# Kernel tuning notes

Hardware: AMD Instinct MI355X
Metric: run time of the kernel (lower is better)

The kernel has to match this reference:

```python
import jax, jax.numpy as jnp
import numpy as np

H = 1024        # hidden_size
V = 50257       # output_size (vocab)
L = 50          # max_length (encoder positions)
N_LAYERS = 2    # python loop count over the shared single-layer GRU


def setup_inputs() -> dict:
    key = jax.random.key(0)
    ks = jax.random.split(key, 16)
    s = 0.02
    return {
        "input_ids": jax.random.randint(ks[0], (1,), 0, V),
        "hidden": jax.random.normal(ks[1], (1, 1, H), jnp.float32),
        "encoder_outputs": jax.random.normal(ks[2], (L, H), jnp.float32),
        # learned parameters
        "emb": jax.random.normal(ks[3], (V, H), jnp.float32) * s,
        "attn_w": jax.random.normal(ks[4], (L, 2 * H), jnp.float32) * s,
        "attn_b": jnp.zeros((L,), jnp.float32),
        "comb_w": jax.random.normal(ks[5], (H, 2 * H), jnp.float32) * s,
        "comb_b": jnp.zeros((H,), jnp.float32),
        "w_ih": jax.random.normal(ks[6], (3 * H, H), jnp.float32) * s,
        "w_hh": jax.random.normal(ks[7], (3 * H, H), jnp.float32) * s,
        "b_ih": jnp.zeros((3 * H,), jnp.float32),
        "b_hh": jnp.zeros((3 * H,), jnp.float32),
        "out_w": jax.random.normal(ks[8], (V, H), jnp.float32) * s,
        "out_b": jnp.zeros((V,), jnp.float32),
    }


def _gru_cell(x, h, w_ih, w_hh, b_ih, b_hh):
    # PyTorch GRU gate order: [r, z, n] stacked along dim 0 of (3H, H) weights.
    gx = w_ih @ x + b_ih
    gh = w_hh @ h + b_hh
    r = jax.nn.sigmoid(gx[:H] + gh[:H])
    z = jax.nn.sigmoid(gx[H:2 * H] + gh[H:2 * H])
    n = jnp.tanh(gx[2 * H:] + r * gh[2 * H:])
    return (1.0 - z) * n + z * h


def reference(input_ids, hidden, encoder_outputs, emb, attn_w, attn_b,
              comb_w, comb_b, w_ih, w_hh, b_ih, b_hh, out_w, out_b):
    # batch=1 single decode step; dropout is identity (eval mode)
    embedded = emb[input_ids[0]]                     # [H]
    h = hidden[0, 0]                                 # [H]
    concat = jnp.concatenate([embedded, h])          # [2H]
    attn_weights = jax.nn.softmax(attn_w @ concat + attn_b)   # [L]
    attn_applied = attn_weights @ encoder_outputs    # [H]  (bmm with batch 1)
    output = comb_w @ jnp.concatenate([embedded, attn_applied]) + comb_b  # [H]
    for _ in range(N_LAYERS):                        # shared-weight GRU called twice
        x = jax.nn.relu(output)
        h = _gru_cell(x, h, w_ih, w_hh, b_ih, b_hh)
        output = h
    log_probs = jax.nn.log_softmax(out_w @ output + out_b)    # [V]
    return log_probs[None, :], h[None, None, :], attn_weights[None, :]
```

## Files before the change

### kernel.cpp

```cpp
#include <hip/hip_runtime.h>
#include <hip/hip_bf16.h>

#define H 1024
#define V 50257
#define L 50

__global__ void attn_kernel(const int* __restrict__ input_ids,
                            const float* __restrict__ hidden,
                            const float* __restrict__ enc,
                            const float* __restrict__ emb,
                            const float* __restrict__ attn_w,
                            const float* __restrict__ attn_b,
                            float* __restrict__ ws_emb,
                            float* __restrict__ ws_app,
                            float* __restrict__ out_attnw) {
    __shared__ __align__(16) float s_concat[2 * H];
    __shared__ float s_w[L];
    const int tid = threadIdx.x;
    const int token = input_ids[0];

    const float4* e4 = (const float4*)(emb + (size_t)token * H);
    const float4* h4 = (const float4*)hidden;
    {
        float4 e = e4[tid];
        float4 h = h4[tid];
        ((float4*)s_concat)[tid] = e;
        ((float4*)(s_concat + H))[tid] = h;
        ((float4*)ws_emb)[tid] = e;
    }
    __syncthreads();

    const int wave = tid >> 6, lane = tid & 63;
    for (int l = wave; l < L; l += 4) {
        const float4* r4 = (const float4*)(attn_w + (size_t)l * 2 * H);
        const float4* c4 = (const float4*)s_concat;
        float acc = 0.f;
        for (int k = lane; k < 512; k += 64) {
            float4 a = r4[k], b = c4[k];
            acc += a.x * b.x + a.y * b.y + a.z * b.z + a.w * b.w;
        }
        #pragma unroll
        for (int off = 32; off; off >>= 1) acc += __shfl_down(acc, off);
        if (lane == 0) s_w[l] = acc + attn_b[l];
    }
    __syncthreads();

    if (tid == 0) {
        float m = s_w[0];
        for (int l = 1; l < L; ++l) m = fmaxf(m, s_w[l]);
        float s = 0.f;
        for (int l = 0; l < L; ++l) { s_w[l] = __expf(s_w[l] - m); s += s_w[l]; }
        float inv = 1.f / s;
        for (int l = 0; l < L; ++l) s_w[l] *= inv;
    }
    __syncthreads();
    if (tid < L) out_attnw[tid] = s_w[tid];

    float4 acc = make_float4(0.f, 0.f, 0.f, 0.f);
    for (int l = 0; l < L; ++l) {
        float w = s_w[l];
        float4 v = ((const float4*)(enc + (size_t)l * H))[tid];
        acc.x += w * v.x; acc.y += w * v.y; acc.z += w * v.z; acc.w += w * v.w;
    }
    ((float4*)ws_app)[tid] = acc;
}

__global__ void comb_kernel(const float* __restrict__ comb_w,
                            const float* __restrict__ comb_b,
                            const float* __restrict__ embedded,
                            const float* __restrict__ applied,
                            float* __restrict__ x1) {
    __shared__ __align__(16) float s_c[2 * H];
    const int tid = threadIdx.x;
    ((float4*)s_c)[tid] = ((const float4*)embedded)[tid];
    ((float4*)(s_c + H))[tid] = ((const float4*)applied)[tid];
    __syncthreads();

    const int wave = tid >> 6, lane = tid & 63;
    const int i = blockIdx.x * 4 + wave;
    const float4* r4 = (const float4*)(comb_w + (size_t)i * 2 * H);
    const float4* c4 = (const float4*)s_c;
    float acc = 0.f;
    for (int k = lane; k < 512; k += 64) {
        float4 a = r4[k], b = c4[k];
        acc += a.x * b.x + a.y * b.y + a.z * b.z + a.w * b.w;
    }
    #pragma unroll
    for (int off = 32; off; off >>= 1) acc += __shfl_down(acc, off);
    if (lane == 0) x1[i] = fmaxf(acc + comb_b[i], 0.f);
}

__global__ void gru_kernel(const float* __restrict__ x,
                           const float* __restrict__ hprev,
                           const float* __restrict__ w_ih,
                           const float* __restrict__ w_hh,
                           const float* __restrict__ b_ih,
                           const float* __restrict__ b_hh,
                           float* __restrict__ h_out,
                           float* __restrict__ x_out,
                           float* __restrict__ h_copy)
{
    __shared__ __align__(16) float s_x[H];
    __shared__ __align__(16) float s_h[H];
    const int tid = threadIdx.x;
    ((float4*)s_x)[tid] = ((const float4*)x)[tid];
    ((float4*)s_h)[tid] = ((const float4*)hprev)[tid];
    __syncthreads();

    const int wave = tid >> 6, lane = tid & 63;
    const int i = blockIdx.x * 4 + wave;
    const float4* x4 = (const float4*)s_x;
    const float4* h4 = (const float4*)s_h;
    const float4* wr_x = (const float4*)(w_ih + (size_t)i * H);
    const float4* wz_x = (const float4*)(w_ih + (size_t)(H + i) * H);
    const float4* wn_x = (const float4*)(w_ih + (size_t)(2 * H + i) * H);
    const float4* wr_h = (const float4*)(w_hh + (size_t)i * H);
    const float4* wz_h = (const float4*)(w_hh + (size_t)(H + i) * H);
    const float4* wn_h = (const float4*)(w_hh + (size_t)(2 * H + i) * H);

    float ar = 0.f, az = 0.f, an = 0.f, br = 0.f, bz = 0.f, bn = 0.f;
    for (int k = lane; k < 256; k += 64) {
        float4 xv = x4[k], hv = h4[k], t;
        t = wr_x[k]; ar += t.x * xv.x + t.y * xv.y + t.z * xv.z + t.w * xv.w;
        t = wz_x[k]; az += t.x * xv.x + t.y * xv.y + t.z * xv.z + t.w * xv.w;
        t = wn_x[k]; an += t.x * xv.x + t.y * xv.y + t.z * xv.z + t.w * xv.w;
        t = wr_h[k]; br += t.x * hv.x + t.y * hv.y + t.z * hv.z + t.w * hv.w;
        t = wz_h[k]; bz += t.x * hv.x + t.y * hv.y + t.z * hv.z + t.w * hv.w;
        t = wn_h[k]; bn += t.x * hv.x + t.y * hv.y + t.z * hv.z + t.w * hv.w;
    }
    #pragma unroll
    for (int off = 32; off; off >>= 1) {
        ar += __shfl_down(ar, off); az += __shfl_down(az, off);
        an += __shfl_down(an, off); br += __shfl_down(br, off);
        bz += __shfl_down(bz, off); bn += __shfl_down(bn, off);
    }
    if (lane == 0) {
        float gxr = ar + b_ih[i],         ghr = br + b_hh[i];
        float gxz = az + b_ih[H + i],     ghz = bz + b_hh[H + i];
        float gxn = an + b_ih[2 * H + i], ghn = bn + b_hh[2 * H + i];
        float r = 1.f / (1.f + expf(-(gxr + ghr)));
        float z = 1.f / (1.f + expf(-(gxz + ghz)));
        float n = tanhf(gxn + r * ghn);
        float hn = (1.f - z) * n + z * s_h[i];
        h_out[i] = hn;
        if (x_out) x_out[i] = fmaxf(hn, 0.f);
        if (h_copy) h_copy[i] = hn;
    }
}

__global__ void logits_kernel(const float* __restrict__ out_w,
                              const float* __restrict__ out_b,
                              const float* __restrict__ h,
                              float* __restrict__ logits,
                              float* __restrict__ partials) {
    __shared__ __align__(16) float s_h[H];
    __shared__ float s_part[4];
    const int tid = threadIdx.x;
    ((float4*)s_h)[tid] = ((const float4*)h)[tid];
    __syncthreads();

    const int wave = tid >> 6, lane = tid & 63;
    const float4* h4 = (const float4*)s_h;
    float psum = 0.f;
    #pragma unroll
    for (int rr = 0; rr < 2; ++rr) {
        const int v = blockIdx.x * 8 + wave * 2 + rr;
        if (v < V) {
            const float4* w4 = (const float4*)(out_w + (size_t)v * H);
            float acc = 0.f;
            for (int k = lane; k < 256; k += 64) {
                float4 a = w4[k], b = h4[k];
                acc += a.x * b.x + a.y * b.y + a.z * b.z + a.w * b.w;
            }
            #pragma unroll
            for (int off = 32; off; off >>= 1) acc += __shfl_down(acc, off);
            if (lane == 0) {
                float lg = acc + out_b[v];
                logits[v] = lg;
                psum += expf(lg);
            }
        }
    }
    if (lane == 0) s_part[wave] = psum;
    __syncthreads();
    if (tid == 0) partials[blockIdx.x] = s_part[0] + s_part[1] + s_part[2] + s_part[3];
}

__global__ void lse_kernel(const float* __restrict__ partials, int n,
                           float* __restrict__ lse) {
    __shared__ float red[256];
    const int tid = threadIdx.x;
    float s = 0.f;
    for (int i = tid; i < n; i += 256) s += partials[i];
    red[tid] = s;
    __syncthreads();
    for (int off = 128; off; off >>= 1) {
        if (tid < off) red[tid] += red[tid + off];
        __syncthreads();
    }
    if (tid == 0) *lse = logf(red[0]);
}

__global__ void sub_kernel(const float* __restrict__ logits,
                           const float* __restrict__ lse,
                           float* __restrict__ out) {
    const int v = blockIdx.x * 256 + threadIdx.x;
    if (v < V) out[v] = logits[v] - *lse;
}

extern "C" void kernel_launch(void* const* d_in, const int* in_sizes, int n_in,
                              void* d_out, int out_size, void* d_ws, size_t ws_size,
                              hipStream_t stream) {
    const int*   input_ids = (const int*)d_in[0];
    const float* hidden    = (const float*)d_in[1];
    const float* enc       = (const float*)d_in[2];
    const float* emb       = (const float*)d_in[3];
    const float* attn_w    = (const float*)d_in[4];
    const float* attn_b    = (const float*)d_in[5];
    const float* comb_w    = (const float*)d_in[6];
    const float* comb_b    = (const float*)d_in[7];
    const float* w_ih      = (const float*)d_in[8];
    const float* w_hh      = (const float*)d_in[9];
    const float* b_ih      = (const float*)d_in[10];
    const float* b_hh      = (const float*)d_in[11];
    const float* out_w     = (const float*)d_in[12];
    const float* out_b     = (const float*)d_in[13];

    float* out = (float*)d_out;
    float* ws  = (float*)d_ws;
    float* ws_emb    = ws;
    float* ws_app    = ws + 1024;
    float* ws_x1     = ws + 2048;
    float* ws_h1     = ws + 3072;
    float* ws_x2     = ws + 4096;
    float* ws_h2     = ws + 5120;
    float* ws_logits = ws + 6144;
    float* ws_part   = ws + 6144 + 50432;
    float* ws_lse    = ws_part + 6400;

    const int nblk_logits = (V + 7) / 8;

    attn_kernel<<<1, 256, 0, stream>>>(input_ids, hidden, enc, emb, attn_w, attn_b,
                                       ws_emb, ws_app, out + V + H);
    comb_kernel<<<256, 256, 0, stream>>>(comb_w, comb_b, ws_emb, ws_app, ws_x1);
    gru_kernel<<<256, 256, 0, stream>>>(ws_x1, hidden, w_ih, w_hh, b_ih, b_hh,
                                        ws_h1, ws_x2, nullptr);
    gru_kernel<<<256, 256, 0, stream>>>(ws_x2, ws_h1, w_ih, w_hh, b_ih, b_hh,
                                        ws_h2, nullptr, out + V);
    logits_kernel<<<nblk_logits, 256, 0, stream>>>(out_w, out_b, ws_h2,
                                                   ws_logits, ws_part);
    lse_kernel<<<1, 256, 0, stream>>>(ws_part, nblk_logits, ws_lse);
    sub_kernel<<<(V + 255) / 256, 256, 0, stream>>>(ws_logits, ws_lse, out);
}
```

Baseline: 451.2 us.

## Fuse decoder step into one persistent kernel with grid barriers

Replaces the seven separate kernels (attention, combine, two GRU steps, logits, logsumexp, subtract) with one persistent 256-block kernel that separates phases with atomic-counter grid barriers. Attention scores are spread over 50 blocks instead of one, and logits are written directly to the output then corrected in place. This removes launch gaps and the single-block attention bottleneck, at the cost of relying on all blocks being co-resident and spin-wait barrier overhead.

```diff
diff --git a/kernel.cpp b/kernel.cpp
--- a/kernel.cpp
+++ b/kernel.cpp
@@ -4,208 +4,222 @@
 #define H 1024
 #define V 50257
 #define L 50
-
-__global__ void attn_kernel(const int* __restrict__ input_ids,
-                            const float* __restrict__ hidden,
-                            const float* __restrict__ enc,
-                            const float* __restrict__ emb,
-                            const float* __restrict__ attn_w,
-                            const float* __restrict__ attn_b,
-                            float* __restrict__ ws_emb,
-                            float* __restrict__ ws_app,
-                            float* __restrict__ out_attnw) {
-    __shared__ __align__(16) float s_concat[2 * H];
-    __shared__ float s_w[L];
-    const int tid = threadIdx.x;
+#define NB 256
+#define NT 1024
+
+__device__ inline void gridbar(unsigned* cnt) {
+    __syncthreads();
+    if (threadIdx.x == 0) {
+        __threadfence();
+        atomicAdd(cnt, 1u);
+        while (__hip_atomic_load(cnt, __ATOMIC_ACQUIRE, __HIP_MEMORY_SCOPE_AGENT) < NB)
+            __builtin_amdgcn_s_sleep(2);
+        __threadfence();
+    }
+    __syncthreads();
+}
+
+__global__ __launch_bounds__(NT, 4) void fused_decoder(
+    const int* __restrict__ input_ids, const float* __restrict__ hidden,
+    const float* __restrict__ enc,     const float* __restrict__ emb,
+    const float* __restrict__ attn_w,  const float* __restrict__ attn_b,
+    const float* __restrict__ comb_w,  const float* __restrict__ comb_b,
+    const float* __restrict__ w_ih,    const float* __restrict__ w_hh,
+    const float* __restrict__ b_ih,    const float* __restrict__ b_hh,
+    const float* __restrict__ out_w,   const float* __restrict__ out_b,
+    float* __restrict__ out, float* __restrict__ ws, unsigned* __restrict__ bar)
+{
+    __shared__ float smem[2048 + 192];
+    const int tid  = threadIdx.x;
+    const int bid  = blockIdx.x;
+    const int wave = tid >> 6, lane = tid & 63;
+
+    float* ws_scores = ws;
+    float* ws_app    = ws + 64;
+    float* ws_x1     = ws_app + H;
+    float* ws_h1     = ws_x1 + H;
+    float* ws_x2     = ws_h1 + H;
+    float* ws_h2     = ws_x2 + H;
+    float* ws_part   = ws_h2 + H;
+
     const int token = input_ids[0];
-
-    const float4* e4 = (const float4*)(emb + (size_t)token * H);
-    const float4* h4 = (const float4*)hidden;
-    {
-        float4 e = e4[tid];
-        float4 h = h4[tid];
-        ((float4*)s_concat)[tid] = e;
-        ((float4*)(s_concat + H))[tid] = h;
-        ((float4*)ws_emb)[tid] = e;
-    }
-    __syncthreads();
-
-    const int wave = tid >> 6, lane = tid & 63;
-    for (int l = wave; l < L; l += 4) {
-        const float4* r4 = (const float4*)(attn_w + (size_t)l * 2 * H);
-        const float4* c4 = (const float4*)s_concat;
+    const float* embrow = emb + (size_t)token * H;
+
+    if (bid < L) {
+        const float* arow = attn_w + (size_t)bid * 2 * H;
         float acc = 0.f;
-        for (int k = lane; k < 512; k += 64) {
-            float4 a = r4[k], b = c4[k];
+        if (tid < 512) {
+            float4 a = ((const float4*)arow)[tid];
+            float4 x = (tid < 256) ? ((const float4*)embrow)[tid]
+                                   : ((const float4*)hidden)[tid - 256];
+            acc = a.x * x.x + a.y * x.y + a.z * x.z + a.w * x.w;
+        }
+        #pragma unroll
+        for (int off = 32; off; off >>= 1) acc += __shfl_down(acc, off);
+        if (tid < 512 && lane == 0) smem[wave] = acc;
+        __syncthreads();
+        if (tid == 0) {
+            float s = 0.f;
+            for (int w = 0; w < 8; ++w) s += smem[w];
+            ws_scores[bid] = s + attn_b[bid];
+        }
+    }
+    gridbar(bar + 0 * 16);
+
+    {
+        if (tid == 0) {
+            float m = ws_scores[0];
+            for (int l = 1; l < L; ++l) m = fmaxf(m, ws_scores[l]);
+            float s = 0.f;
+            for (int l = 0; l < L; ++l) { float e = expf(ws_scores[l] - m); smem[l] = e; s += e; }
+            float inv = 1.f / s;
+            for (int l = 0; l < L; ++l) smem[l] *= inv;
+        }
+        __syncthreads();
+        if (tid < 4) {
+            int j = bid * 4 + tid;
+            float acc = 0.f;
+            for (int l = 0; l < L; ++l) acc += smem[l] * enc[l * H + j];
+            ws_app[j] = acc;
+        }
+        if (bid == 0 && tid >= 64 && tid < 64 + L)
+            out[V + H + (tid - 64)] = smem[tid - 64];
+    }
+    gridbar(bar + 1 * 16);
+
+    {
+        float4* sc4 = (float4*)smem;
+        if (tid < 256)      sc4[tid]       = ((const float4*)embrow)[tid];
+        else if (tid < 512) sc4[tid]       = ((const float4*)ws_app)[tid - 256];
+        __syncthreads();
+        int r = bid * 4 + (wave >> 2);
+        int seg = wave & 3;
+        const float4* wr = (const float4*)(comb_w + (size_t)r * 2 * H);
+        float acc = 0.f;
+        #pragma unroll
+        for (int k = 0; k < 2; ++k) {
+            int idx = seg * 128 + k * 64 + lane;
+            float4 a = wr[idx], b = sc4[idx];
             acc += a.x * b.x + a.y * b.y + a.z * b.z + a.w * b.w;
         }
         #pragma unroll
         for (int off = 32; off; off >>= 1) acc += __shfl_down(acc, off);
-        if (lane == 0) s_w[l] = acc + attn_b[l];
-    }
-    __syncthreads();
-
-    if (tid == 0) {
-        float m = s_w[0];
-        for (int l = 1; l < L; ++l) m = fmaxf(m, s_w[l]);
-        float s = 0.f;
-        for (int l = 0; l < L; ++l) { s_w[l] = __expf(s_w[l] - m); s += s_w[l]; }
-        float inv = 1.f / s;
-        for (int l = 0; l < L; ++l) s_w[l] *= inv;
-    }
-    __syncthreads();
-    if (tid < L) out_attnw[tid] = s_w[tid];
-
-    float4 acc = make_float4(0.f, 0.f, 0.f, 0.f);
-    for (int l = 0; l < L; ++l) {
-        float w = s_w[l];
-        float4 v = ((const float4*)(enc + (size_t)l * H))[tid];
-        acc.x += w * v.x; acc.y += w * v.y; acc.z += w * v.z; acc.w += w * v.w;
-    }
-    ((float4*)ws_app)[tid] = acc;
-}
-
-__global__ void comb_kernel(const float* __restrict__ comb_w,
-                            const float* __restrict__ comb_b,
-                            const float* __restrict__ embedded,
-                            const float* __restrict__ applied,
-                            float* __restrict__ x1) {
-    __shared__ __align__(16) float s_c[2 * H];
-    const int tid = threadIdx.x;
-    ((float4*)s_c)[tid] = ((const float4*)embedded)[tid];
-    ((float4*)(s_c + H))[tid] = ((const float4*)applied)[tid];
-    __syncthreads();
-
-    const int wave = tid >> 6, lane = tid & 63;
-    const int i = blockIdx.x * 4 + wave;
-    const float4* r4 = (const float4*)(comb_w + (size_t)i * 2 * H);
-    const float4* c4 = (const float4*)s_c;
-    float acc = 0.f;
-    for (int k = lane; k < 512; k += 64) {
-        float4 a = r4[k], b = c4[k];
-        acc += a.x * b.x + a.y * b.y + a.z * b.z + a.w * b.w;
-    }
-    #pragma unroll
-    for (int off = 32; off; off >>= 1) acc += __shfl_down(acc, off);
-    if (lane == 0) x1[i] = fmaxf(acc + comb_b[i], 0.f);
-}
-
-__global__ void gru_kernel(const float* __restrict__ x,
-                           const float* __restrict__ hprev,
-                           const float* __restrict__ w_ih,
-                           const float* __restrict__ w_hh,
-                           const float* __restrict__ b_ih,
-                           const float* __restrict__ b_hh,
-                           float* __restrict__ h_out,
-                           float* __restrict__ x_out,
-                           float* __restrict__ h_copy)
-{
-    __shared__ __align__(16) float s_x[H];
-    __shared__ __align__(16) float s_h[H];
-    const int tid = threadIdx.x;
-    ((float4*)s_x)[tid] = ((const float4*)x)[tid];
-    ((float4*)s_h)[tid] = ((const float4*)hprev)[tid];
-    __syncthreads();
-
-    const int wave = tid >> 6, lane = tid & 63;
-    const int i = blockIdx.x * 4 + wave;
-    const float4* x4 = (const float4*)s_x;
-    const float4* h4 = (const float4*)s_h;
-    const float4* wr_x = (const float4*)(w_ih + (size_t)i * H);
-    const float4* wz_x = (const float4*)(w_ih + (size_t)(H + i) * H);
-    const float4* wn_x = (const float4*)(w_ih + (size_t)(2 * H + i) * H);
-    const float4* wr_h = (const float4*)(w_hh + (size_t)i * H);
-    const float4* wz_h = (const float4*)(w_hh + (size_t)(H + i) * H);
-    const float4* wn_h = (const float4*)(w_hh + (size_t)(2 * H + i) * H);
-
-    float ar = 0.f, az = 0.f, an = 0.f, br = 0.f, bz = 0.f, bn = 0.f;
-    for (int k = lane; k < 256; k += 64) {
-        float4 xv = x4[k], hv = h4[k], t;
-        t = wr_x[k]; ar += t.x * xv.x + t.y * xv.y + t.z * xv.z + t.w * xv.w;
-        t = wz_x[k]; az += t.x * xv.x + t.y * xv.y + t.z * xv.z + t.w * xv.w;
-        t = wn_x[k]; an += t.x * xv.x + t.y * xv.y + t.z * xv.z + t.w * xv.w;
-        t = wr_h[k]; br += t.x * hv.x + t.y * hv.y + t.z * hv.z + t.w * hv.w;
-        t = wz_h[k]; bz += t.x * hv.x + t.y * hv.y + t.z * hv.z + t.w * hv.w;
-        t = wn_h[k]; bn += t.x * hv.x + t.y * hv.y + t.z * hv.z + t.w * hv.w;
-    }
-    #pragma unroll
-    for (int off = 32; off; off >>= 1) {
-        ar += __shfl_down(ar, off); az += __shfl_down(az, off);
-        an += __shfl_down(an, off); br += __shfl_down(br, off);
-        bz += __shfl_down(bz, off); bn += __shfl_down(bn, off);
-    }
-    if (lane == 0) {
-        float gxr = ar + b_ih[i],         ghr = br + b_hh[i];
-        float gxz = az + b_ih[H + i],     ghz = bz + b_hh[H + i];
-        float gxn = an + b_ih[2 * H + i], ghn = bn + b_hh[2 * H + i];
-        float r = 1.f / (1.f + expf(-(gxr + ghr)));
-        float z = 1.f / (1.f + expf(-(gxz + ghz)));
-        float n = tanhf(gxn + r * ghn);
-        float hn = (1.f - z) * n + z * s_h[i];
-        h_out[i] = hn;
-        if (x_out) x_out[i] = fmaxf(hn, 0.f);
-        if (h_copy) h_copy[i] = hn;
-    }
-}
-
-__global__ void logits_kernel(const float* __restrict__ out_w,
-                              const float* __restrict__ out_b,
-                              const float* __restrict__ h,
-                              float* __restrict__ logits,
-                              float* __restrict__ partials) {
-    __shared__ __align__(16) float s_h[H];
-    __shared__ float s_part[4];
-    const int tid = threadIdx.x;
-    ((float4*)s_h)[tid] = ((const float4*)h)[tid];
-    __syncthreads();
-
-    const int wave = tid >> 6, lane = tid & 63;
-    const float4* h4 = (const float4*)s_h;
-    float psum = 0.f;
-    #pragma unroll
-    for (int rr = 0; rr < 2; ++rr) {
-        const int v = blockIdx.x * 8 + wave * 2 + rr;
-        if (v < V) {
-            const float4* w4 = (const float4*)(out_w + (size_t)v * H);
+        if (lane == 0) smem[2048 + wave] = acc;
+        __syncthreads();
+        if (tid < 4) {
+            int rr = bid * 4 + tid;
+            float s = smem[2048 + tid * 4] + smem[2048 + tid * 4 + 1]
+                    + smem[2048 + tid * 4 + 2] + smem[2048 + tid * 4 + 3];
+            ws_x1[rr] = fmaxf(s + comb_b[rr], 0.f);
+        }
+    }
+    gridbar(bar + 2 * 16);
+
+    for (int layer = 0; layer < 2; ++layer) {
+        const float* x  = (layer == 0) ? ws_x1 : ws_x2;
+        const float* hp = (layer == 0) ? hidden : ws_h1;
+        float* h_out  = (layer == 0) ? ws_h1 : ws_h2;
+        float* x_out  = (layer == 0) ? ws_x2 : nullptr;
+        float* h_copy = (layer == 0) ? nullptr : out + V;
+
+        float4* sx4 = (float4*)smem;
+        float4* sh4 = (float4*)(smem + 1024);
+        if (tid < 256)      sx4[tid]       = ((const float4*)x)[tid];
+        else if (tid < 512) sh4[tid - 256] = ((const float4*)hp)[tid - 256];
+        __syncthreads();
+
+        int r   = bid * 4 + (wave >> 2);
+        int seg = wave & 3;
+        int idx = seg * 64 + lane;
+        float4 xv = sx4[idx], hv = sh4[idx];
+        const float4* m0 = (const float4*)(w_ih + (size_t)r * H);
+        const float4* m1 = (const float4*)(w_ih + (size_t)(H + r) * H);
+        const float4* m2 = (const float4*)(w_ih + (size_t)(2 * H + r) * H);
+        const float4* m3 = (const float4*)(w_hh + (size_t)r * H);
+        const float4* m4 = (const float4*)(w_hh + (size_t)(H + r) * H);
+        const float4* m5 = (const float4*)(w_hh + (size_t)(2 * H + r) * H);
+        float4 t;
+        float a0, a1, a2, a3, a4, a5;
+        t = m0[idx]; a0 = t.x * xv.x + t.y * xv.y + t.z * xv.z + t.w * xv.w;
+        t = m1[idx]; a1 = t.x * xv.x + t.y * xv.y + t.z * xv.z + t.w * xv.w;
+        t = m2[idx]; a2 = t.x * xv.x + t.y * xv.y + t.z * xv.z + t.w * xv.w;
+        t = m3[idx]; a3 = t.x * hv.x + t.y * hv.y + t.z * hv.z + t.w * hv.w;
+        t = m4[idx]; a4 = t.x * hv.x + t.y * hv.y + t.z * hv.z + t.w * hv.w;
+        t = m5[idx]; a5 = t.x * hv.x + t.y * hv.y + t.z * hv.z + t.w * hv.w;
+        #pragma unroll
+        for (int off = 32; off; off >>= 1) {
+            a0 += __shfl_down(a0, off); a1 += __shfl_down(a1, off);
+            a2 += __shfl_down(a2, off); a3 += __shfl_down(a3, off);
+            a4 += __shfl_down(a4, off); a5 += __shfl_down(a5, off);
+        }
+        if (lane == 0) {
+            float* p = smem + 2048 + wave * 8;
+            p[0] = a0; p[1] = a1; p[2] = a2; p[3] = a3; p[4] = a4; p[5] = a5;
+        }
+        __syncthreads();
+        if (tid < 4) {
+            int rr = bid * 4 + tid;
+            float g0 = 0, g1 = 0, g2 = 0, g3 = 0, g4 = 0, g5 = 0;
+            #pragma unroll
+            for (int s = 0; s < 4; ++s) {
+                float* p = smem + 2048 + (tid * 4 + s) * 8;
+                g0 += p[0]; g1 += p[1]; g2 += p[2]; g3 += p[3]; g4 += p[4]; g5 += p[5];
+            }
+            float gxr = g0 + b_ih[rr],         ghr = g3 + b_hh[rr];
+            float gxz = g1 + b_ih[H + rr],     ghz = g4 + b_hh[H + rr];
+            float gxn = g2 + b_ih[2 * H + rr], ghn = g5 + b_hh[2 * H + rr];
+            float rg = 1.f / (1.f + expf(-(gxr + ghr)));
+            float zg = 1.f / (1.f + expf(-(gxz + ghz)));
+            float ng = tanhf(gxn + rg * ghn);
+            float hval = smem[1024 + rr];
+            float hn = (1.f - zg) * ng + zg * hval;
+            h_out[rr] = hn;
+            if (x_out)  x_out[rr]  = fmaxf(hn, 0.f);
+            if (h_copy) h_copy[rr] = hn;
+        }
+        gridbar(bar + (3 + layer) * 16);
+    }
+
+    {
+        float4* sh4 = (float4*)smem;
+        if (tid < 256) sh4[tid] = ((const float4*)ws_h2)[tid];
+        __syncthreads();
+        int gw = bid * 16 + wave;
+        float psum = 0.f;
+        for (int v = gw; v < V; v += 4096) {
+            const float4* wr = (const float4*)(out_w + (size_t)v * H);
             float acc = 0.f;
-            for (int k = lane; k < 256; k += 64) {
-                float4 a = w4[k], b = h4[k];
+            #pragma unroll
+            for (int k = 0; k < 4; ++k) {
+                int idx = k * 64 + lane;
+                float4 a = wr[idx], b = sh4[idx];
                 acc += a.x * b.x + a.y * b.y + a.z * b.z + a.w * b.w;
             }
             #pragma unroll
             for (int off = 32; off; off >>= 1) acc += __shfl_down(acc, off);
             if (lane == 0) {
                 float lg = acc + out_b[v];
-                logits[v] = lg;
+                out[v] = lg;
                 psum += expf(lg);
             }
         }
-    }
-    if (lane == 0) s_part[wave] = psum;
-    __syncthreads();
-    if (tid == 0) partials[blockIdx.x] = s_part[0] + s_part[1] + s_part[2] + s_part[3];
-}
-
-__global__ void lse_kernel(const float* __restrict__ partials, int n,
-                           float* __restrict__ lse) {
-    __shared__ float red[256];
-    const int tid = threadIdx.x;
-    float s = 0.f;
-    for (int i = tid; i < n; i += 256) s += partials[i];
-    red[tid] = s;
-    __syncthreads();
-    for (int off = 128; off; off >>= 1) {
-        if (tid < off) red[tid] += red[tid + off];
-        __syncthreads();
-    }
-    if (tid == 0) *lse = logf(red[0]);
-}
-
-__global__ void sub_kernel(const float* __restrict__ logits,
-                           const float* __restrict__ lse,
-                           float* __restrict__ out) {
-    const int v = blockIdx.x * 256 + threadIdx.x;
-    if (v < V) out[v] = logits[v] - *lse;
+        if (lane == 0) ws_part[gw] = psum;
+    }
+    gridbar(bar + 5 * 16);
+
+    {
+        float s = 0.f;
+        for (int i = tid; i < 4096; i += NT) s += ws_part[i];
+        smem[tid] = s;
+        __syncthreads();
+        for (int off = 512; off; off >>= 1) {
+            if (tid < off) smem[tid] += smem[tid + off];
+            __syncthreads();
+        }
+        float lse = logf(smem[0]);
+        int g = bid * NT + tid;
+        if (g < V) out[g] -= lse;
+    }
 }
 
 extern "C" void kernel_launch(void* const* d_in, const int* in_sizes, int n_in,
@@ -228,27 +242,10 @@
 
     float* out = (float*)d_out;
     float* ws  = (float*)d_ws;
-    float* ws_emb    = ws;
-    float* ws_app    = ws + 1024;
-    float* ws_x1     = ws + 2048;
-    float* ws_h1     = ws + 3072;
-    float* ws_x2     = ws + 4096;
-    float* ws_h2     = ws + 5120;
-    float* ws_logits = ws + 6144;
-    float* ws_part   = ws + 6144 + 50432;
-    float* ws_lse    = ws_part + 6400;
-
-    const int nblk_logits = (V + 7) / 8;
-
-    attn_kernel<<<1, 256, 0, stream>>>(input_ids, hidden, enc, emb, attn_w, attn_b,
-                                       ws_emb, ws_app, out + V + H);
-    comb_kernel<<<256, 256, 0, stream>>>(comb_w, comb_b, ws_emb, ws_app, ws_x1);
-    gru_kernel<<<256, 256, 0, stream>>>(ws_x1, hidden, w_ih, w_hh, b_ih, b_hh,
-                                        ws_h1, ws_x2, nullptr);
-    gru_kernel<<<256, 256, 0, stream>>>(ws_x2, ws_h1, w_ih, w_hh, b_ih, b_hh,
-                                        ws_h2, nullptr, out + V);
-    logits_kernel<<<nblk_logits, 256, 0, stream>>>(out_w, out_b, ws_h2,
-                                                   ws_logits, ws_part);
-    lse_kernel<<<1, 256, 0, stream>>>(ws_part, nblk_logits, ws_lse);
-    sub_kernel<<<(V + 255) / 256, 256, 0, stream>>>(ws_logits, ws_lse, out);
+    unsigned* bar = (unsigned*)(ws + 64 + 5 * 1024 + 4096);
+
+    hipMemsetAsync(bar, 0, 6 * 16 * sizeof(unsigned), stream);
+    fused_decoder<<<NB, NT, 0, stream>>>(input_ids, hidden, enc, emb, attn_w, attn_b,
+                                         comb_w, comb_b, w_ih, w_hh, b_ih, b_hh,
+                                         out_w, out_b, out, ws, bar);
 }
```

Result: slower. 535.7 us (+18.7%).
